# Optimization experiments

Hardware: AMD Instinct MI355X
Metric: run time of the kernel (lower is better)

Reference implementation:

```python
import jax, jax.numpy as jnp
import numpy as np

W, B, S, D = 4, 1, 1024, 1024   # simulated world_size, batch, local seq, embed_dim
H, DS, HM = 16, 64, 4            # num_heads, summary_dim, meta_heads


def mha(q, k, v, w_in, b_in, w_out, b_out, nheads):
    """torch nn.MultiheadAttention (batch_first). Returns (out, head-averaged weights)."""
    d = q.shape[-1]
    hd = d // nheads
    wq, wk, wv = jnp.split(w_in, 3, axis=0)
    bq, bk, bv = jnp.split(b_in, 3)
    Bq, Sq, _ = q.shape
    Sk = k.shape[1]
    qh = (q @ wq.T + bq).reshape(Bq, Sq, nheads, hd)
    kh = (k @ wk.T + bk).reshape(Bq, Sk, nheads, hd)
    vh = (v @ wv.T + bv).reshape(Bq, Sk, nheads, hd)
    scores = jnp.einsum('bqhd,bkhd->bhqk', qh, kh) / float(np.sqrt(hd))
    attn = jax.nn.softmax(scores, axis=-1)
    out = jnp.einsum('bhqk,bkhd->bqhd', attn, vh).reshape(Bq, Sq, d)
    return out @ w_out.T + b_out, attn.mean(axis=1)


def attn_stats(attn):
    """attn: (B, S) -> (B, 4) [entropy, gini, max, top5]."""
    ent = -(attn * jnp.log(attn + 1e-8)).sum(-1, keepdims=True)
    s = jnp.sort(attn, axis=-1)
    n = attn.shape[-1]
    idx = jnp.arange(1, n + 1, dtype=attn.dtype)
    gini = 2.0 * (idx * s).sum(-1) / (n * s.sum(-1) + 1e-8) - (n + 1) / n
    mx = attn.max(-1, keepdims=True)
    k = min(5, n)
    top5 = jax.lax.top_k(attn, k)[0].sum(-1, keepdims=True)
    return jnp.concatenate([ent, gini[..., None], mx, top5], axis=-1)


def _forward(x, local_in_w, local_in_b, local_out_w, local_out_b,
             sum_query, sum_in_w, sum_in_b, sum_out_w, sum_out_b,
             pat_w1, pat_b1, pat_w2, pat_b2, comb_w, comb_b,
             meta_in_w, meta_in_b, meta_out_w, meta_out_b,
             route_w1, route_b1, route_w2, route_b2,
             cross_in_w, cross_in_b, cross_out_w, cross_out_b,
             gate_w, gate_b, proj_w, proj_b):
    nW = x.shape[0]

    # 1) local attention per rank: (W,B,S,D)
    local = jax.vmap(lambda xc: mha(xc, xc, xc, local_in_w, local_in_b,
                                    local_out_w, local_out_b, H)[0])(x)

    # 2) chunk summary per rank
    def summarize(lo):
        q = jnp.broadcast_to(sum_query, (lo.shape[0], 1, lo.shape[-1]))
        content, w = mha(q, lo, lo, sum_in_w, sum_in_b, sum_out_w, sum_out_b, H)
        content, w = content[:, 0], w[:, 0]              # (B,D), (B,S)
        pat = attn_stats(w)                               # (B,4)
        pat = jax.nn.relu(pat @ pat_w1.T + pat_b1) @ pat_w2.T + pat_b2
        return jnp.concatenate([content, pat], axis=-1) @ comb_w.T + comb_b

    summaries = jax.vmap(summarize)(local)                # (W,B,DS)
    all_sum = jnp.transpose(summaries, (1, 0, 2))         # (B,W,DS) = all-gather

    # 3) meta attention over chunk summaries -> routing weights
    refined, chunk_attn = mha(all_sum, all_sum, all_sum,
                              meta_in_w, meta_in_b, meta_out_w, meta_out_b, HM)
    logits = (jax.nn.relu(refined @ route_w1.T + route_b1) @ route_w2.T + route_b2)[..., 0]
    routing = jax.nn.softmax(logits, axis=-1)             # (B,W)

    all_chunks = jnp.transpose(local, (1, 0, 2, 3))       # (B,W,S,D) = all-gather

    # 4) selective cross-attention + gated combine, per rank
    def per_rank(r, lo):
        rm = routing * (1.0 - jax.nn.one_hot(r, nW, dtype=routing.dtype))
        rm = rm / (rm.sum(-1, keepdims=True) + 1e-8)
        kv = jnp.einsum('bw,bwsd->bsd', rm, all_chunks)
        cross, _ = mha(lo, kv, kv, cross_in_w, cross_in_b, cross_out_w, cross_out_b, H)
        g = jax.nn.sigmoid(jnp.concatenate([lo, cross], axis=-1) @ gate_w.T + gate_b)
        comb = g * cross + (1.0 - g) * lo
        return comb @ proj_w.T + proj_b

    out = jax.vmap(per_rank)(jnp.arange(nW), local)       # (W,B,S,D)
    return out


def setup_inputs() -> dict:
    key = jax.random.key(0)
    ks = iter(jax.random.split(key, 40))
    p = lambda *shape: jax.random.normal(next(ks), shape, dtype=jnp.float32) * 0.02
    inp = {
        'x': jax.random.normal(next(ks), (W, B, S, D), dtype=jnp.float32),
        'local_in_w': p(3 * D, D), 'local_in_b': p(3 * D),
        'local_out_w': p(D, D), 'local_out_b': p(D),
        'sum_query': p(1, 1, D),
        'sum_in_w': p(3 * D, D), 'sum_in_b': p(3 * D),
        'sum_out_w': p(D, D), 'sum_out_b': p(D),
        'pat_w1': p(DS, 4), 'pat_b1': p(DS),
        'pat_w2': p(DS, DS), 'pat_b2': p(DS),
        'comb_w': p(DS, D + DS), 'comb_b': p(DS),
        'meta_in_w': p(3 * DS, DS), 'meta_in_b': p(3 * DS),
        'meta_out_w': p(DS, DS), 'meta_out_b': p(DS),
        'route_w1': p(DS, DS), 'route_b1': p(DS),
        'route_w2': p(1, DS), 'route_b2': p(1),
        'cross_in_w': p(3 * D, D), 'cross_in_b': p(3 * D),
        'cross_out_w': p(D, D), 'cross_out_b': p(D),
        'gate_w': p(D, 2 * D), 'gate_b': p(D),
        'proj_w': p(D, D), 'proj_b': p(D),
    }
    return inp


def reference(x, local_in_w, local_in_b, local_out_w, local_out_b,
              sum_query, sum_in_w, sum_in_b, sum_out_w, sum_out_b,
              pat_w1, pat_b1, pat_w2, pat_b2, comb_w, comb_b,
              meta_in_w, meta_in_b, meta_out_w, meta_out_b,
              route_w1, route_b1, route_w2, route_b2,
              cross_in_w, cross_in_b, cross_out_w, cross_out_b,
              gate_w, gate_b, proj_w, proj_b):
    return _forward(x, local_in_w, local_in_b, local_out_w, local_out_b,
                    sum_query, sum_in_w, sum_in_b, sum_out_w, sum_out_b,
                    pat_w1, pat_b1, pat_w2, pat_b2, comb_w, comb_b,
                    meta_in_w, meta_in_b, meta_out_w, meta_out_b,
                    route_w1, route_b1, route_w2, route_b2,
                    cross_in_w, cross_in_b, cross_out_w, cross_out_b,
                    gate_w, gate_b, proj_w, proj_b)
```

## Files before the change

### kernel.cpp

```cpp
#include <hip/hip_runtime.h>
#include <hip/hip_bf16.h>
#include <stdint.h>

typedef uint16_t u16;
typedef __attribute__((ext_vector_type(8))) short short8;
typedef __attribute__((ext_vector_type(4))) short short4v;
typedef __attribute__((ext_vector_type(8))) unsigned short ushort8;
typedef __attribute__((ext_vector_type(4))) float f32x4;

#define AS1 __attribute__((address_space(1)))
#define AS3 __attribute__((address_space(3)))

__device__ __forceinline__ float b2f(u16 u){
  union{uint32_t i; float f;} v; v.i=((uint32_t)u)<<16; return v.f;
}
__device__ __forceinline__ u16 f2b(float f){
  union{uint32_t i; float f;} v; v.f=f;
  return (u16)((v.i + 0x7fffu + ((v.i>>16)&1u))>>16);
}
__device__ __forceinline__ u16 f2bf(float f){
  __hip_bfloat16 h = __float2bfloat16(f);
  return *reinterpret_cast<u16*>(&h);
}

struct CvtP { const float* src[8]; u16* dst[8]; long n[8]; };
__global__ void cvt_multi(CvtP p) {
  const int seg = blockIdx.y;
  const long i = ((long)blockIdx.x*256 + threadIdx.x)*8;
  if (i >= p.n[seg]) return;
  const float* in = p.src[seg];
  float4 a = *(const float4*)&in[i];
  float4 b = *(const float4*)&in[i+4];
  ushort8 o;
  o[0]=f2b(a.x); o[1]=f2b(a.y); o[2]=f2b(a.z); o[3]=f2b(a.w);
  o[4]=f2b(b.x); o[5]=f2b(b.y); o[6]=f2b(b.z); o[7]=f2b(b.w);
  *(ushort8*)&p.dst[seg][i] = o;
}

struct GemmP {
  const u16* A; const u16* B; u16* C; const float* bias;
  const u16* B2; u16* C2; const float* bias2;
  long lda, ldb, ldc, ldb2, ldc2;
  int K, Nstore, Nstore2, ySplit, act, outf;
  float scale;
};

__global__ __launch_bounds__(512) void gemm_nt(GemmP p) {
  __shared__ __align__(16) u16 lA[2][4096];
  __shared__ __align__(16) u16 lB[2][4096];
  const int t = threadIdx.x;
  const int wave = t >> 6, lane = t & 63;
  int by = blockIdx.y;
  const u16* Bp; u16* Cp; const float* bias; long ldb, ldc; int nst;
  if (by >= p.ySplit) {
    by -= p.ySplit; Bp = p.B2; Cp = p.C2; bias = p.bias2;
    ldb = p.ldb2; ldc = p.ldc2; nst = p.Nstore2;
  } else {
    Bp = p.B; Cp = p.C; bias = p.bias; ldb = p.ldb; ldc = p.ldc; nst = p.Nstore;
  }
  const u16* A = p.A + (long)blockIdx.x * 128 * p.lda;
  const u16* B = Bp + (long)by * 128 * ldb;
  const int srow = t >> 2, skk = (t & 3) * 8;
  const int wr = wave >> 2, wc = wave & 3;
  const int fr = lane & 15, fk = (lane >> 4) * 8;
  f32x4 acc[4][2] = {};

  __builtin_amdgcn_global_load_lds((const AS1 void*)(A + (long)srow*p.lda + skk),
                                   (AS3 void*)&lA[0][t*8], 16, 0, 0);
  __builtin_amdgcn_global_load_lds((const AS1 void*)(B + (long)srow*ldb + skk),
                                   (AS3 void*)&lB[0][t*8], 16, 0, 0);
  __syncthreads();
  int cur = 0;
  for (int k0 = 0; k0 < p.K; k0 += 32) {
    if (k0 + 32 < p.K) {
      const int nb = cur ^ 1, kn = k0 + 32;
      __builtin_amdgcn_global_load_lds((const AS1 void*)(A + (long)srow*p.lda + kn + skk),
                                       (AS3 void*)&lA[nb][t*8], 16, 0, 0);
      __builtin_amdgcn_global_load_lds((const AS1 void*)(B + (long)srow*ldb + kn + skk),
                                       (AS3 void*)&lB[nb][t*8], 16, 0, 0);
    }
    short8 av[4], bv[2];
    #pragma unroll
    for (int mi = 0; mi < 4; ++mi) av[mi] = *(const short8*)&lA[cur][(wr*64 + mi*16 + fr)*32 + fk];
    #pragma unroll
    for (int ni = 0; ni < 2; ++ni) bv[ni] = *(const short8*)&lB[cur][(wc*32 + ni*16 + fr)*32 + fk];
    #pragma unroll
    for (int mi = 0; mi < 4; ++mi)
      #pragma unroll
      for (int ni = 0; ni < 2; ++ni)
        acc[mi][ni] = __builtin_amdgcn_mfma_f32_16x16x32_bf16(av[mi], bv[ni], acc[mi][ni], 0, 0, 0);
    __syncthreads();
    cur ^= 1;
  }

  const int rbase = blockIdx.x*128 + wr*64;
  const int cbase = by*128 + wc*32;
  const int rsub = (lane >> 4) * 4;
  #pragma unroll
  for (int ni = 0; ni < 2; ++ni) {
    const int col = cbase + ni*16 + fr;
    if (col >= nst) continue;
    const float bs = bias ? bias[col] : 0.f;
    #pragma unroll
    for (int mi = 0; mi < 4; ++mi) {
      #pragma unroll
      for (int j = 0; j < 4; ++j) {
        float v = acc[mi][ni][j] * p.scale + bs;
        if (p.act == 1) v = 1.f / (1.f + __expf(-v));
        const long idx = (long)(rbase + mi*16 + rsub + j) * ldc + col;
        if (p.outf) ((float*)Cp)[idx] = v;
        else        Cp[idx] = f2b(v);
      }
    }
  }
}

struct FlashP {
  const u16 *q, *k, *v; u16* o;
  long ldq, ldkv, ldo;
  long qB, kvB, oB;
};

__global__ __launch_bounds__(256) void flash_k(FlashP p) {
  const int t = threadIdx.x, w4 = t >> 6, lane = t & 63;
  const int qt = blockIdx.x, h = blockIdx.y, wz = blockIdx.z;
  const int fr = lane & 15, g = lane >> 4, fk = g * 8;
  __shared__ __align__(16) u16 kt[64][72];
  __shared__ __align__(16) u16 vt[64][72];
  __shared__ __align__(16) u16 pl[4][16][72];

  const u16* Q = p.q + (long)wz*p.qB + (long)(qt*64 + w4*16)*p.ldq + h*64;
  const u16* K = p.k + (long)wz*p.kvB + h*64;
  const u16* V = p.v + (long)wz*p.kvB + h*64;

  short8 aq[2];
  aq[0] = *(const short8*)&Q[(long)fr*p.ldq + fk];
  aq[1] = *(const short8*)&Q[(long)fr*p.ldq + 32 + fk];

  f32x4 acc[4] = {};
  float ml = -3e38f, ll = 0.f;
  const float C = 0.125f * 1.44269504f;

  const int krow = t >> 2, kseg = (t & 3) * 16;
  const int vp = t & 31, vc = (t >> 5) * 8;

  short8 kr0, kr1, vr0, vr1;
  kr0 = *(const short8*)&K[(long)krow*p.ldkv + kseg];
  kr1 = *(const short8*)&K[(long)krow*p.ldkv + kseg + 8];
  vr0 = *(const short8*)&V[(long)(2*vp)*p.ldkv + vc];
  vr1 = *(const short8*)&V[(long)(2*vp + 1)*p.ldkv + vc];

  for (int it = 0; it < 16; ++it) {
    *(short8*)&kt[krow][kseg]     = kr0;
    *(short8*)&kt[krow][kseg + 8] = kr1;
    #pragma unroll
    for (int e = 0; e < 8; ++e) {
      const uint32_t pk = (uint32_t)(uint16_t)vr0[e] | ((uint32_t)(uint16_t)vr1[e] << 16);
      *(uint32_t*)&vt[vc + e][2*vp] = pk;
    }
    __syncthreads();

    if (it + 1 < 16) {
      const int kn = (it + 1) * 64;
      kr0 = *(const short8*)&K[(long)(kn + krow)*p.ldkv + kseg];
      kr1 = *(const short8*)&K[(long)(kn + krow)*p.ldkv + kseg + 8];
      vr0 = *(const short8*)&V[(long)(kn + 2*vp)*p.ldkv + vc];
      vr1 = *(const short8*)&V[(long)(kn + 2*vp + 1)*p.ldkv + vc];
    }

    f32x4 s[4] = {};
    __builtin_amdgcn_s_setprio(1);
    #pragma unroll
    for (int ni = 0; ni < 4; ++ni) {
      short8 bk0 = *(const short8*)&kt[ni*16 + fr][fk];
      short8 bk1 = *(const short8*)&kt[ni*16 + fr][32 + fk];
      s[ni] = __builtin_amdgcn_mfma_f32_16x16x32_bf16(bk0, aq[0], s[ni], 0, 0, 0);
      s[ni] = __builtin_amdgcn_mfma_f32_16x16x32_bf16(bk1, aq[1], s[ni], 0, 0, 0);
    }
    __builtin_amdgcn_s_setprio(0);

    float rm = s[0][0];
    #pragma unroll
    for (int ni = 0; ni < 4; ++ni)
      #pragma unroll
      for (int j = 0; j < 4; ++j) rm = fmaxf(rm, s[ni][j]);
    rm = fmaxf(rm, __shfl_xor(rm, 16, 64));
    rm = fmaxf(rm, __shfl_xor(rm, 32, 64));
    const float rml = rm * C;

    if (__any(rml > ml + 11.5f)) {
      const float mnl = fmaxf(ml, rml);
      const float al = exp2f(ml - mnl);
      const float a0 = __shfl(al, g*4 + 0, 64);
      const float a1 = __shfl(al, g*4 + 1, 64);
      const float a2 = __shfl(al, g*4 + 2, 64);
      const float a3 = __shfl(al, g*4 + 3, 64);
      #pragma unroll
      for (int nv = 0; nv < 4; ++nv) {
        acc[nv][0] *= a0; acc[nv][1] *= a1; acc[nv][2] *= a2; acc[nv][3] *= a3;
      }
      ll *= al;
      ml = mnl;
    }

    float rs = 0.f;
    u16 pb[4][4];
    #pragma unroll
    for (int ni = 0; ni < 4; ++ni)
      #pragma unroll
      for (int j = 0; j < 4; ++j) {
        const float pv = exp2f(s[ni][j]*C - ml);
        rs += pv;
        pb[ni][j] = f2bf(pv);
      }
    rs += __shfl_xor(rs, 16, 64);
    rs += __shfl_xor(rs, 32, 64);
    ll += rs;

    #pragma unroll
    for (int ni = 0; ni < 4; ++ni) {
      short4v pk4;
      pk4[0] = (short)pb[ni][0]; pk4[1] = (short)pb[ni][1];
      pk4[2] = (short)pb[ni][2]; pk4[3] = (short)pb[ni][3];
      *(short4v*)&pl[w4][fr][ni*16 + g*4] = pk4;
    }

    __builtin_amdgcn_s_setprio(1);
    #pragma unroll
    for (int ks = 0; ks < 2; ++ks) {
      short8 pa = *(const short8*)&pl[w4][fr][ks*32 + fk];
      #pragma unroll
      for (int nv = 0; nv < 4; ++nv) {
        short8 bvv = *(const short8*)&vt[nv*16 + fr][ks*32 + fk];
        acc[nv] = __builtin_amdgcn_mfma_f32_16x16x32_bf16(pa, bvv, acc[nv], 0, 0, 0);
      }
    }
    __builtin_amdgcn_s_setprio(0);
    __syncthreads();
  }

  const float l0 = __shfl(ll, g*4 + 0, 64);
  const float l1 = __shfl(ll, g*4 + 1, 64);
  const float l2 = __shfl(ll, g*4 + 2, 64);
  const float l3 = __shfl(ll, g*4 + 3, 64);
  const float inv[4] = {1.f/l0, 1.f/l1, 1.f/l2, 1.f/l3};
  u16* O = p.o + (long)wz*p.oB + (long)(qt*64 + w4*16)*p.ldo + h*64;
  #pragma unroll
  for (int j = 0; j < 4; ++j)
    #pragma unroll
    for (int nv = 0; nv < 4; ++nv)
      O[(long)(g*4 + j)*p.ldo + nv*16 + fr] = f2bf(acc[nv][j] * inv[j]);
}

__global__ void gemv_qs(const float* sq, const float* w, const float* b, float* out) {
  const int t = threadIdx.x, nl = t & 63, kq = t >> 6;
  const int n = blockIdx.x*64 + nl;
  const float* row = w + (long)n * 1024 + kq*256;
  const float* q = sq + kq*256;
  float s = 0.f;
  for (int k = 0; k < 256; k += 4) {
    float4 ww = *(const float4*)&row[k];
    float4 qq = *(const float4*)&q[k];
    s += qq.x*ww.x + qq.y*ww.y + qq.z*ww.z + qq.w*ww.w;
  }
  __shared__ float ps[4][64];
  ps[kq][nl] = s;
  __syncthreads();
  if (t < 64) out[blockIdx.x*64 + t] = ps[0][t]+ps[1][t]+ps[2][t]+ps[3][t] + b[blockIdx.x*64 + t];
}

__global__ void sum_attend(const float* qs, const u16* sumkv, float* content, float* pall) {
  const int h = blockIdx.x, w = blockIdx.y, t = threadIdx.x;
  const int lane = t & 63, wv = t >> 6;
  __shared__ float qsh[64];
  __shared__ float sc[1024];
  __shared__ float rmax[4], rsum[4];
  __shared__ float po[4][64];
  if (t < 64) qsh[t] = qs[h*64 + t];
  __syncthreads();
  const u16* kbase = sumkv + (long)w*2097152 + h*64;
  float e[4];
  float mx = -1e30f;
  #pragma unroll
  for (int j = 0; j < 4; ++j) {
    const int k = j*256 + t;
    const u16* krow = kbase + (long)k * 2048;
    float s = 0.f;
    #pragma unroll
    for (int d = 0; d < 64; d += 8) {
      ushort8 kk = *(const ushort8*)&krow[d];
      #pragma unroll
      for (int q = 0; q < 8; ++q) s += qsh[d+q] * b2f(kk[q]);
    }
    s *= 0.125f;
    e[j] = s;
    mx = fmaxf(mx, s);
  }
  #pragma unroll
  for (int o = 32; o; o >>= 1) mx = fmaxf(mx, __shfl_xor(mx, o, 64));
  if (lane == 0) rmax[wv] = mx;
  __syncthreads();
  mx = fmaxf(fmaxf(rmax[0],rmax[1]), fmaxf(rmax[2],rmax[3]));
  float sum = 0.f;
  #pragma unroll
  for (int j = 0; j < 4; ++j) { e[j] = __expf(e[j]-mx); sum += e[j]; }
  #pragma unroll
  for (int o = 32; o; o >>= 1) sum += __shfl_xor(sum, o, 64);
  if (lane == 0) rsum[wv] = sum;
  __syncthreads();
  const float inv = 1.f / (rsum[0]+rsum[1]+rsum[2]+rsum[3]);
  float* pr = pall + ((long)w*16 + h)*1024;
  #pragma unroll
  for (int j = 0; j < 4; ++j) {
    const int k = j*256 + t;
    const float pn = e[j]*inv;
    sc[k] = pn;
    pr[k] = pn;
  }
  __syncthreads();
  const u16* vbase = sumkv + (long)w*2097152 + 1024 + h*64;
  float o = 0.f;
  const int k0 = wv*256;
  for (int k = k0; k < k0+256; ++k) o += sc[k] * b2f(vbase[(long)k*2048 + lane]);
  po[wv][lane] = o;
  __syncthreads();
  if (t < 64) content[(long)w*1024 + h*64 + t] = po[0][t]+po[1][t]+po[2][t]+po[3][t];
}

__global__ void wavg_k(const float* pall, float* wavg) {
  const int w = blockIdx.y, k = blockIdx.x*256 + threadIdx.x;
  float s = 0.f;
  #pragma unroll
  for (int h = 0; h < 16; ++h) s += pall[((long)w*16 + h)*1024 + k];
  wavg[w*1024 + k] = s * (1.f/16.f);
}

__global__ void contproj_k(const float* content, const float* w_, const float* b, float* out) {
  const int w = blockIdx.y, t = threadIdx.x;
  const int nl = t & 63, kq = t >> 6;
  const int n = blockIdx.x*64 + nl;
  const float* c = content + w*1024 + kq*256;
  const float* row = w_ + (long)n * 1024 + kq*256;
  float s = 0.f;
  for (int k = 0; k < 256; k += 4) {
    float4 ww = *(const float4*)&row[k];
    s += c[k]*ww.x + c[k+1]*ww.y + c[k+2]*ww.z + c[k+3]*ww.w;
  }
  __shared__ float ps[4][64];
  ps[kq][nl] = s;
  __syncthreads();
  if (t < 64) out[w*1024 + blockIdx.x*64 + t] = ps[0][t]+ps[1][t]+ps[2][t]+ps[3][t] + b[blockIdx.x*64 + t];
}

__global__ void stats1_k(const float* wavg, float* part) {
  const int c = blockIdx.x, w = blockIdx.y, t = threadIdx.x;
  __shared__ float a[1024];
  for (int i = t; i < 1024; i += 256) a[i] = wavg[w*1024 + i];
  __syncthreads();
  const int jl = t & 63, iq = t >> 6;
  const int j = c*64 + jl;
  const float aj = a[j];
  int pr = 0;
  const int i0 = iq*256;
  #pragma unroll 8
  for (int i = i0; i < i0+256; ++i) {
    const float ai = a[i];
    pr += (ai < aj) || (ai == aj && i < j);
  }
  __shared__ int prs[4][64];
  prs[iq][jl] = pr;
  __syncthreads();
  if (t < 64) {
    const int rank = 1 + prs[0][jl] + prs[1][jl] + prs[2][jl] + prs[3][jl];
    float ent = -aj * logf(aj + 1e-8f);
    float gnum = (float)rank * aj;
    float ssum = aj;
    float mx = aj;
    float top5 = (rank >= 1020) ? aj : 0.f;
    #pragma unroll
    for (int o = 32; o; o >>= 1) {
      ent += __shfl_xor(ent, o, 64);
      gnum += __shfl_xor(gnum, o, 64);
      ssum += __shfl_xor(ssum, o, 64);
      mx = fmaxf(mx, __shfl_xor(mx, o, 64));
      top5 += __shfl_xor(top5, o, 64);
    }
    if (t == 0) {
      float* pp = part + ((w*16 + c) * 5);
      pp[0]=ent; pp[1]=gnum; pp[2]=ssum; pp[3]=mx; pp[4]=top5;
    }
  }
}

__global__ void stats2_k(const float* part, float* stats) {
  const int w = blockIdx.x, t = threadIdx.x;
  const int c = t & 15, stat = t >> 4;
  float v = 0.f;
  const bool active = stat < 5;
  if (active) v = part[(w*16 + c)*5 + stat];
  #pragma unroll
  for (int o = 8; o; o >>= 1) {
    const float ov = __shfl_xor(v, o, 64);
    v = (stat == 3) ? fmaxf(v, ov) : (v + ov);
  }
  __shared__ float r5[5];
  if (active && c == 0) r5[stat] = v;
  __syncthreads();
  if (t == 0) {
    stats[w*4+0] = r5[0];
    stats[w*4+1] = 2.f*r5[1]/(1024.f*r5[2] + 1e-8f) - 1025.f/1024.f;
    stats[w*4+2] = r5[3];
    stats[w*4+3] = r5[4];
  }
}

__global__ void patsum_k(const float* stats, const float* contprj,
                         const float* pw1, const float* pb1, const float* pw2, const float* pb2,
                         const float* combw, const float* combb, float* summ) {
  const int w = blockIdx.x, t = threadIdx.x;
  const int nl = t & 63, kq = t >> 6;
  __shared__ float p1[64], pat[64];
  __shared__ float ps[4][64];
  __shared__ float ps2[4][64];
  if (t < 64) {
    float s = 0.f;
    #pragma unroll
    for (int k = 0; k < 4; ++k) s += stats[w*4+k] * pw1[t*4+k];
    p1[t] = fmaxf(s + pb1[t], 0.f);
  }
  __syncthreads();
  {
    float s = 0.f;
    const float* rw = pw2 + (long)nl*64 + kq*16;
    const float* pp = p1 + kq*16;
    #pragma unroll
    for (int k = 0; k < 16; ++k) s += pp[k] * rw[k];
    ps[kq][nl] = s;
  }
  __syncthreads();
  if (t < 64) pat[t] = ps[0][t]+ps[1][t]+ps[2][t]+ps[3][t] + pb2[t];
  __syncthreads();
  const float* c = contprj + w*1024;
  const float* row = combw + (long)nl * 1088;
  float s = 0.f;
  const int k0 = kq*272;
  for (int k = k0; k < k0+272; ++k) {
    const float rv = row[k];
    const float cv = (k < 1024) ? c[k] : pat[k-1024];
    s += cv * rv;
  }
  ps2[kq][nl] = s;
  __syncthreads();
  if (t < 64) summ[w*64 + t] = ps2[0][t]+ps2[1][t]+ps2[2][t]+ps2[3][t] + combb[t];
}

__global__ void meta_k(const float* summ, const float* miw, const float* mib,
                       const float* mow, const float* mob, const float* rw1, const float* rb1,
                       const float* rw2, const float* rb2, float* routing) {
  const int t = threadIdx.x;
  __shared__ float qkv[4][192];
  __shared__ float sc[64];
  __shared__ float o[4][64];
  __shared__ float rf[4][64];
  __shared__ float t1[4][64];
  __shared__ float lg[4];
  for (int idx = t; idx < 768; idx += 64) {
    const int w = idx / 192, rrow = idx % 192;
    const float* rw = miw + (long)rrow * 64;
    float s = 0.f;
    for (int k = 0; k < 64; ++k) s += summ[w*64+k] * rw[k];
    qkv[w][rrow] = s + mib[rrow];
  }
  __syncthreads();
  {
    const int h = t >> 4, i = (t >> 2) & 3, j = t & 3;
    float s = 0.f;
    #pragma unroll
    for (int d = 0; d < 16; ++d) s += qkv[i][h*16+d] * qkv[j][64 + h*16+d];
    sc[t] = s * 0.25f;
  }
  __syncthreads();
  if (t < 16) {
    const float a0=sc[t*4], a1=sc[t*4+1], a2=sc[t*4+2], a3=sc[t*4+3];
    const float m = fmaxf(fmaxf(a0,a1), fmaxf(a2,a3));
    const float e0=__expf(a0-m), e1=__expf(a1-m), e2=__expf(a2-m), e3=__expf(a3-m);
    const float s = e0+e1+e2+e3;
    sc[t*4]=e0/s; sc[t*4+1]=e1/s; sc[t*4+2]=e2/s; sc[t*4+3]=e3/s;
  }
  __syncthreads();
  for (int idx = t; idx < 256; idx += 64) {
    const int i = idx >> 6, c = idx & 63, h = c >> 4;
    float s = 0.f;
    #pragma unroll
    for (int j = 0; j < 4; ++j) s += sc[(h*4+i)*4+j] * qkv[j][128 + c];
    o[i][c] = s;
  }
  __syncthreads();
  for (int idx = t; idx < 256; idx += 64) {
    const int i = idx >> 6, n = idx & 63;
    const float* rw = mow + (long)n * 64;
    float s = 0.f;
    for (int k = 0; k < 64; ++k) s += o[i][k] * rw[k];
    rf[i][n] = s + mob[n];
  }
  __syncthreads();
  for (int idx = t; idx < 256; idx += 64) {
    const int i = idx >> 6, n = idx & 63;
    const float* rw = rw1 + (long)n * 64;
    float s = 0.f;
    for (int k = 0; k < 64; ++k) s += rf[i][k] * rw[k];
    t1[i][n] = fmaxf(s + rb1[n], 0.f);
  }
  __syncthreads();
  if (t < 4) {
    float s = 0.f;
    for (int k = 0; k < 64; ++k) s += t1[t][k] * rw2[k];
    lg[t] = s + rb2[0];
  }
  __syncthreads();
  if (t == 0) {
    const float m = fmaxf(fmaxf(lg[0],lg[1]), fmaxf(lg[2],lg[3]));
    float e[4], s = 0.f;
    #pragma unroll
    for (int i = 0; i < 4; ++i) { e[i] = __expf(lg[i]-m); s += e[i]; }
    #pragma unroll
    for (int i = 0; i < 4; ++i) routing[i] = e[i]/s;
  }
}

__global__ void kvr_k(const u16* local, const float* routing, u16* kvr) {
  const int r = blockIdx.y;
  const long e = ((long)blockIdx.x*256 + threadIdx.x) * 8;
  float rm[4]; float s = 0.f;
  #pragma unroll
  for (int w = 0; w < 4; ++w) { rm[w] = (w == r) ? 0.f : routing[w]; s += rm[w]; }
  const float inv = 1.f / (s + 1e-8f);
  ushort8 a0 = *(const ushort8*)&local[e];
  ushort8 a1 = *(const ushort8*)&local[1048576 + e];
  ushort8 a2 = *(const ushort8*)&local[2097152 + e];
  ushort8 a3 = *(const ushort8*)&local[3145728 + e];
  ushort8 out;
  #pragma unroll
  for (int j = 0; j < 8; ++j)
    out[j] = f2b((rm[0]*b2f(a0[j]) + rm[1]*b2f(a1[j]) + rm[2]*b2f(a2[j]) + rm[3]*b2f(a3[j])) * inv);
  *(ushort8*)&kvr[(long)r*1048576 + e] = out;
}

__global__ void gcat_k(const u16* local, const u16* cross, u16* gcat) {
  const long e = ((long)blockIdx.x*256 + threadIdx.x) * 8;
  const long row = e >> 11, col = e & 2047;
  const u16* src = (col < 1024) ? &local[row*1024 + col] : &cross[row*1024 + col - 1024];
  *(ushort8*)&gcat[e] = *(const ushort8*)src;
}

__global__ void comb_k(const u16* g, const u16* cross, const u16* local, u16* comb) {
  const long e = ((long)blockIdx.x*256 + threadIdx.x) * 8;
  ushort8 gg = *(const ushort8*)&g[e];
  ushort8 cc = *(const ushort8*)&cross[e];
  ushort8 ll = *(const ushort8*)&local[e];
  ushort8 out;
  #pragma unroll
  for (int j = 0; j < 8; ++j) {
    const float gf = b2f(gg[j]);
    out[j] = f2b(gf*b2f(cc[j]) + (1.f-gf)*b2f(ll[j]));
  }
  *(ushort8*)&comb[e] = out;
}

static void gemm1(hipStream_t st, dim3 grid,
                  const u16* A, long lda, const u16* B, long ldb,
                  u16* C, long ldc, const float* bias,
                  int K, int N, float scale, int act, int outf) {
  GemmP p = {};
  p.A=A; p.B=B; p.C=C; p.bias=bias;
  p.lda=lda; p.ldb=ldb; p.ldc=ldc;
  p.K=K; p.Nstore=N; p.ySplit=1<<30; p.act=act; p.outf=outf; p.scale=scale;
  gemm_nt<<<grid, dim3(512), 0, st>>>(p);
}

extern "C" void kernel_launch(void* const* d_in, const int* in_sizes, int n_in,
                              void* d_out, int out_size, void* d_ws, size_t ws_size,
                              hipStream_t stream) {
  (void)in_sizes; (void)n_in; (void)out_size; (void)ws_size;
  const float* x   = (const float*)d_in[0];
  const float* liw = (const float*)d_in[1];
  const float* lib = (const float*)d_in[2];
  const float* low = (const float*)d_in[3];
  const float* lob = (const float*)d_in[4];
  const float* sq  = (const float*)d_in[5];
  const float* siw = (const float*)d_in[6];
  const float* sib = (const float*)d_in[7];
  const float* sow = (const float*)d_in[8];
  const float* sob = (const float*)d_in[9];
  const float* pw1 = (const float*)d_in[10];
  const float* pb1 = (const float*)d_in[11];
  const float* pw2 = (const float*)d_in[12];
  const float* pb2 = (const float*)d_in[13];
  const float* cbw = (const float*)d_in[14];
  const float* cbb = (const float*)d_in[15];
  const float* miw = (const float*)d_in[16];
  const float* mib = (const float*)d_in[17];
  const float* mow = (const float*)d_in[18];
  const float* mob = (const float*)d_in[19];
  const float* rw1 = (const float*)d_in[20];
  const float* rb1 = (const float*)d_in[21];
  const float* rw2 = (const float*)d_in[22];
  const float* rb2 = (const float*)d_in[23];
  const float* ciw = (const float*)d_in[24];
  const float* cib = (const float*)d_in[25];
  const float* cow = (const float*)d_in[26];
  const float* cob = (const float*)d_in[27];
  const float* gw  = (const float*)d_in[28];
  const float* gb  = (const float*)d_in[29];
  const float* pw  = (const float*)d_in[30];
  const float* pb  = (const float*)d_in[31];

  char* ws = (char*)d_ws;
  u16* qkv    = (u16*)(ws + 0);
  u16* aout   = (u16*)(ws + 25165824);
  u16* local  = (u16*)(ws + 33554432);
  u16* scratch= (u16*)(ws + 41943040);
  u16* s2048  = (u16*)(ws + 79691776);
  u16* cq     = (u16*)(ws + 96468992);
  u16* kvr    = (u16*)(ws + 104857600);
  u16* crossb = (u16*)(ws + 113246208);
  char* sf = ws + 121634816;
  float* qs      = (float*)(sf + 0);
  float* pall    = (float*)(sf + 4096);
  float* wavg    = (float*)(sf + 266240);
  float* content = (float*)(sf + 282624);
  float* contprj = (float*)(sf + 299008);
  float* stats   = (float*)(sf + 315392);
  float* summ    = (float*)(sf + 315456);
  float* routing = (float*)(sf + 316480);
  float* part    = (float*)(sf + 316544);
  u16* siwkvb = (u16*)(ws + 122028032);
  u16* lowb   = (u16*)(ws + 126222336);
  u16* ciwb   = (u16*)(ws + 128319488);
  u16* cowb   = (u16*)(ws + 134610944);
  u16* gwb    = (u16*)(ws + 136708096);
  u16* pwb    = (u16*)(ws + 140902400);
  u16* xb   = crossb;
  u16* liwb = scratch;

  CvtP cp;
  cp.src[0]=x;   cp.dst[0]=xb;     cp.n[0]=4194304;
  cp.src[1]=liw; cp.dst[1]=liwb;   cp.n[1]=3145728;
  cp.src[2]=low; cp.dst[2]=lowb;   cp.n[2]=1048576;
  cp.src[3]=siw+1048576; cp.dst[3]=siwkvb; cp.n[3]=2097152;
  cp.src[4]=ciw; cp.dst[4]=ciwb;   cp.n[4]=3145728;
  cp.src[5]=cow; cp.dst[5]=cowb;   cp.n[5]=1048576;
  cp.src[6]=gw;  cp.dst[6]=gwb;    cp.n[6]=2097152;
  cp.src[7]=pw;  cp.dst[7]=pwb;    cp.n[7]=1048576;
  cvt_multi<<<dim3(2048, 8), dim3(256), 0, stream>>>(cp);

  gemm1(stream, dim3(32,24), xb,1024, liwb,1024, qkv,3072, lib, 1024, 3072, 1.f, 0, 0);

  {
    FlashP fp;
    fp.q = qkv; fp.k = qkv + 1024; fp.v = qkv + 2048; fp.o = aout;
    fp.ldq = 3072; fp.ldkv = 3072; fp.ldo = 1024;
    fp.qB = 3145728; fp.kvB = 3145728; fp.oB = 1048576;
    flash_k<<<dim3(16,16,4), dim3(256), 0, stream>>>(fp);
  }

  gemm1(stream, dim3(32,8), aout,1024, lowb,1024, local,1024, lob, 1024, 1024, 1.f, 0, 0);

  {
    GemmP p = {};
    p.A = local; p.lda = 1024; p.K = 1024; p.scale = 1.f;
    p.B = ciwb;   p.C = cq;    p.bias = cib;      p.ldb = 1024; p.ldc = 1024; p.Nstore = 1024;
    p.B2 = siwkvb; p.C2 = s2048; p.bias2 = sib+1024; p.ldb2 = 1024; p.ldc2 = 2048; p.Nstore2 = 2048;
    p.ySplit = 8;
    gemm_nt<<<dim3(32,24), dim3(512), 0, stream>>>(p);
  }

  gemv_qs<<<dim3(16), dim3(256), 0, stream>>>(sq, siw, sib, qs);
  sum_attend<<<dim3(16,4), dim3(256), 0, stream>>>(qs, s2048, content, pall);
  wavg_k<<<dim3(4,4), dim3(256), 0, stream>>>(pall, wavg);
  contproj_k<<<dim3(16,4), dim3(256), 0, stream>>>(content, sow, sob, contprj);
  stats1_k<<<dim3(16,4), dim3(256), 0, stream>>>(wavg, part);
  stats2_k<<<dim3(4), dim3(128), 0, stream>>>(part, stats);
  patsum_k<<<dim3(4), dim3(256), 0, stream>>>(stats, contprj, pw1, pb1, pw2, pb2, cbw, cbb, summ);

  meta_k<<<dim3(1), dim3(64), 0, stream>>>(summ, miw, mib, mow, mob, rw1, rb1, rw2, rb2, routing);

  kvr_k<<<dim3(512,4), dim3(256), 0, stream>>>(local, routing, kvr);

  gemm1(stream, dim3(32,16), kvr,1024, ciwb+1048576,1024, s2048,2048, cib+1024, 1024, 2048, 1.f, 0, 0);

  {
    FlashP fp;
    fp.q = cq; fp.k = s2048; fp.v = s2048 + 1024; fp.o = aout;
    fp.ldq = 1024; fp.ldkv = 2048; fp.ldo = 1024;
    fp.qB = 1048576; fp.kvB = 2097152; fp.oB = 1048576;
    flash_k<<<dim3(16,16,4), dim3(256), 0, stream>>>(fp);
  }

  gemm1(stream, dim3(32,8), aout,1024, cowb,1024, crossb,1024, cob, 1024, 1024, 1.f, 0, 0);

  gcat_k<<<dim3(4096), dim3(256), 0, stream>>>(local, crossb, s2048);
  gemm1(stream, dim3(32,8), s2048,2048, gwb,2048, cq,1024, gb, 2048, 1024, 1.f, 1, 0);

  comb_k<<<dim3(2048), dim3(256), 0, stream>>>(cq, crossb, local, kvr);

  gemm1(stream, dim3(32,8), kvr,1024, pwb,1024, (u16*)d_out,1024, pb, 1024, 1024, 1.f, 0, 1);
}
```

Measured before the change: 433.2 us.

## Fuse gate concat and combine into GEMM; process two query fragments per flash wave

The gate GEMM now reads its two K-halves straight from the local and cross buffers, so the concat kernel is no longer needed. A new epilogue mode applies the sigmoid and the gated blend of cross and local in place, which removes the separate combine kernel and its round trips through memory. Separately, each flash-attention wave now handles 32 query rows (two 16-row fragments), so each K/V tile loaded into LDS is reused twice and the grid is halved. The cost is higher register pressure in the attention kernel and fewer blocks per launch.

```diff
diff --git a/kernel.cpp b/kernel.cpp
--- a/kernel.cpp
+++ b/kernel.cpp
@@ -40,6 +40,7 @@
 struct GemmP {
   const u16* A; const u16* B; u16* C; const float* bias;
   const u16* B2; u16* C2; const float* bias2;
+  const u16* A2; const u16* lr; const u16* cr;
   long lda, ldb, ldc, ldb2, ldc2;
   int K, Nstore, Nstore2, ySplit, act, outf;
   float scale;
@@ -58,39 +59,43 @@
   } else {
     Bp = p.B; Cp = p.C; bias = p.bias; ldb = p.ldb; ldc = p.ldc; nst = p.Nstore;
   }
-  const u16* A = p.A + (long)blockIdx.x * 128 * p.lda;
   const u16* B = Bp + (long)by * 128 * ldb;
   const int srow = t >> 2, skk = (t & 3) * 8;
   const int wr = wave >> 2, wc = wave & 3;
   const int fr = lane & 15, fk = (lane >> 4) * 8;
   f32x4 acc[4][2] = {};
 
-  __builtin_amdgcn_global_load_lds((const AS1 void*)(A + (long)srow*p.lda + skk),
-                                   (AS3 void*)&lA[0][t*8], 16, 0, 0);
-  __builtin_amdgcn_global_load_lds((const AS1 void*)(B + (long)srow*ldb + skk),
-                                   (AS3 void*)&lB[0][t*8], 16, 0, 0);
-  __syncthreads();
+  const int nseg = p.A2 ? 2 : 1;
   int cur = 0;
-  for (int k0 = 0; k0 < p.K; k0 += 32) {
-    if (k0 + 32 < p.K) {
-      const int nb = cur ^ 1, kn = k0 + 32;
-      __builtin_amdgcn_global_load_lds((const AS1 void*)(A + (long)srow*p.lda + kn + skk),
-                                       (AS3 void*)&lA[nb][t*8], 16, 0, 0);
-      __builtin_amdgcn_global_load_lds((const AS1 void*)(B + (long)srow*ldb + kn + skk),
-                                       (AS3 void*)&lB[nb][t*8], 16, 0, 0);
-    }
-    short8 av[4], bv[2];
-    #pragma unroll
-    for (int mi = 0; mi < 4; ++mi) av[mi] = *(const short8*)&lA[cur][(wr*64 + mi*16 + fr)*32 + fk];
-    #pragma unroll
-    for (int ni = 0; ni < 2; ++ni) bv[ni] = *(const short8*)&lB[cur][(wc*32 + ni*16 + fr)*32 + fk];
-    #pragma unroll
-    for (int mi = 0; mi < 4; ++mi)
-      #pragma unroll
-      for (int ni = 0; ni < 2; ++ni)
-        acc[mi][ni] = __builtin_amdgcn_mfma_f32_16x16x32_bf16(av[mi], bv[ni], acc[mi][ni], 0, 0, 0);
+  for (int seg = 0; seg < nseg; ++seg) {
+    const u16* A = (seg ? p.A2 : p.A) + (long)blockIdx.x * 128 * p.lda;
+    const u16* Bs = B + (long)seg * p.K;
+    __builtin_amdgcn_global_load_lds((const AS1 void*)(A + (long)srow*p.lda + skk),
+                                     (AS3 void*)&lA[cur][t*8], 16, 0, 0);
+    __builtin_amdgcn_global_load_lds((const AS1 void*)(Bs + (long)srow*ldb + skk),
+                                     (AS3 void*)&lB[cur][t*8], 16, 0, 0);
     __syncthreads();
-    cur ^= 1;
+    for (int k0 = 0; k0 < p.K; k0 += 32) {
+      if (k0 + 32 < p.K) {
+        const int nb = cur ^ 1, kn = k0 + 32;
+        __builtin_amdgcn_global_load_lds((const AS1 void*)(A + (long)srow*p.lda + kn + skk),
+                                         (AS3 void*)&lA[nb][t*8], 16, 0, 0);
+        __builtin_amdgcn_global_load_lds((const AS1 void*)(Bs + (long)srow*ldb + kn + skk),
+                                         (AS3 void*)&lB[nb][t*8], 16, 0, 0);
+      }
+      short8 av[4], bv[2];
+      #pragma unroll
+      for (int mi = 0; mi < 4; ++mi) av[mi] = *(const short8*)&lA[cur][(wr*64 + mi*16 + fr)*32 + fk];
+      #pragma unroll
+      for (int ni = 0; ni < 2; ++ni) bv[ni] = *(const short8*)&lB[cur][(wc*32 + ni*16 + fr)*32 + fk];
+      #pragma unroll
+      for (int mi = 0; mi < 4; ++mi)
+        #pragma unroll
+        for (int ni = 0; ni < 2; ++ni)
+          acc[mi][ni] = __builtin_amdgcn_mfma_f32_16x16x32_bf16(av[mi], bv[ni], acc[mi][ni], 0, 0, 0);
+      __syncthreads();
+      cur ^= 1;
+    }
   }
 
   const int rbase = blockIdx.x*128 + wr*64;
@@ -106,10 +111,17 @@
       #pragma unroll
       for (int j = 0; j < 4; ++j) {
         float v = acc[mi][ni][j] * p.scale + bs;
-        if (p.act == 1) v = 1.f / (1.f + __expf(-v));
         const long idx = (long)(rbase + mi*16 + rsub + j) * ldc + col;
-        if (p.outf) ((float*)Cp)[idx] = v;
-        else        Cp[idx] = f2b(v);
+        if (p.act == 2) {
+          const float gv = 1.f / (1.f + __expf(-v));
+          const float cv = b2f(p.cr[idx]);
+          const float lv = b2f(p.lr[idx]);
+          Cp[idx] = f2b(gv*cv + (1.f - gv)*lv);
+        } else {
+          if (p.act == 1) v = 1.f / (1.f + __expf(-v));
+          if (p.outf) ((float*)Cp)[idx] = v;
+          else        Cp[idx] = f2b(v);
+        }
       }
     }
   }
@@ -127,18 +139,21 @@
   const int fr = lane & 15, g = lane >> 4, fk = g * 8;
   __shared__ __align__(16) u16 kt[64][72];
   __shared__ __align__(16) u16 vt[64][72];
-  __shared__ __align__(16) u16 pl[4][16][72];
-
-  const u16* Q = p.q + (long)wz*p.qB + (long)(qt*64 + w4*16)*p.ldq + h*64;
+  __shared__ __align__(16) u16 pl[4][32][72];
+
+  const u16* Q = p.q + (long)wz*p.qB + (long)(qt*128 + w4*32)*p.ldq + h*64;
   const u16* K = p.k + (long)wz*p.kvB + h*64;
   const u16* V = p.v + (long)wz*p.kvB + h*64;
 
-  short8 aq[2];
-  aq[0] = *(const short8*)&Q[(long)fr*p.ldq + fk];
-  aq[1] = *(const short8*)&Q[(long)fr*p.ldq + 32 + fk];
-
-  f32x4 acc[4] = {};
-  float ml = -3e38f, ll = 0.f;
+  short8 aq[2][2];
+  #pragma unroll
+  for (int f = 0; f < 2; ++f) {
+    aq[f][0] = *(const short8*)&Q[(long)(f*16 + fr)*p.ldq + fk];
+    aq[f][1] = *(const short8*)&Q[(long)(f*16 + fr)*p.ldq + 32 + fk];
+  }
+
+  f32x4 acc[2][4] = {};
+  float ml[2] = {-3e38f, -3e38f}, ll[2] = {0.f, 0.f};
   const float C = 0.125f * 1.44269504f;
 
   const int krow = t >> 2, kseg = (t & 3) * 16;
@@ -168,88 +183,100 @@
       vr1 = *(const short8*)&V[(long)(kn + 2*vp + 1)*p.ldkv + vc];
     }
 
-    f32x4 s[4] = {};
+    f32x4 s[2][4] = {};
     __builtin_amdgcn_s_setprio(1);
     #pragma unroll
     for (int ni = 0; ni < 4; ++ni) {
       short8 bk0 = *(const short8*)&kt[ni*16 + fr][fk];
       short8 bk1 = *(const short8*)&kt[ni*16 + fr][32 + fk];
-      s[ni] = __builtin_amdgcn_mfma_f32_16x16x32_bf16(bk0, aq[0], s[ni], 0, 0, 0);
-      s[ni] = __builtin_amdgcn_mfma_f32_16x16x32_bf16(bk1, aq[1], s[ni], 0, 0, 0);
+      #pragma unroll
+      for (int f = 0; f < 2; ++f) {
+        s[f][ni] = __builtin_amdgcn_mfma_f32_16x16x32_bf16(bk0, aq[f][0], s[f][ni], 0, 0, 0);
+        s[f][ni] = __builtin_amdgcn_mfma_f32_16x16x32_bf16(bk1, aq[f][1], s[f][ni], 0, 0, 0);
+      }
     }
     __builtin_amdgcn_s_setprio(0);
 
-    float rm = s[0][0];
-    #pragma unroll
-    for (int ni = 0; ni < 4; ++ni)
-      #pragma unroll
-      for (int j = 0; j < 4; ++j) rm = fmaxf(rm, s[ni][j]);
-    rm = fmaxf(rm, __shfl_xor(rm, 16, 64));
-    rm = fmaxf(rm, __shfl_xor(rm, 32, 64));
-    const float rml = rm * C;
-
-    if (__any(rml > ml + 11.5f)) {
-      const float mnl = fmaxf(ml, rml);
-      const float al = exp2f(ml - mnl);
-      const float a0 = __shfl(al, g*4 + 0, 64);
-      const float a1 = __shfl(al, g*4 + 1, 64);
-      const float a2 = __shfl(al, g*4 + 2, 64);
-      const float a3 = __shfl(al, g*4 + 3, 64);
-      #pragma unroll
-      for (int nv = 0; nv < 4; ++nv) {
-        acc[nv][0] *= a0; acc[nv][1] *= a1; acc[nv][2] *= a2; acc[nv][3] *= a3;
+    #pragma unroll
+    for (int f = 0; f < 2; ++f) {
+      float rm = s[f][0][0];
+      #pragma unroll
+      for (int ni = 0; ni < 4; ++ni)
+        #pragma unroll
+        for (int j = 0; j < 4; ++j) rm = fmaxf(rm, s[f][ni][j]);
+      rm = fmaxf(rm, __shfl_xor(rm, 16, 64));
+      rm = fmaxf(rm, __shfl_xor(rm, 32, 64));
+      const float rml = rm * C;
+
+      if (__any(rml > ml[f] + 11.5f)) {
+        const float mnl = fmaxf(ml[f], rml);
+        const float al = exp2f(ml[f] - mnl);
+        const float a0 = __shfl(al, g*4 + 0, 64);
+        const float a1 = __shfl(al, g*4 + 1, 64);
+        const float a2 = __shfl(al, g*4 + 2, 64);
+        const float a3 = __shfl(al, g*4 + 3, 64);
+        #pragma unroll
+        for (int nv = 0; nv < 4; ++nv) {
+          acc[f][nv][0] *= a0; acc[f][nv][1] *= a1;
+          acc[f][nv][2] *= a2; acc[f][nv][3] *= a3;
+        }
+        ll[f] *= al;
+        ml[f] = mnl;
       }
-      ll *= al;
-      ml = mnl;
-    }
-
-    float rs = 0.f;
-    u16 pb[4][4];
-    #pragma unroll
-    for (int ni = 0; ni < 4; ++ni)
-      #pragma unroll
-      for (int j = 0; j < 4; ++j) {
-        const float pv = exp2f(s[ni][j]*C - ml);
-        rs += pv;
-        pb[ni][j] = f2bf(pv);
+
+      float rs = 0.f;
+      u16 pb[4][4];
+      #pragma unroll
+      for (int ni = 0; ni < 4; ++ni)
+        #pragma unroll
+        for (int j = 0; j < 4; ++j) {
+          const float pv = exp2f(s[f][ni][j]*C - ml[f]);
+          rs += pv;
+          pb[ni][j] = f2bf(pv);
+        }
+      rs += __shfl_xor(rs, 16, 64);
+      rs += __shfl_xor(rs, 32, 64);
+      ll[f] += rs;
+
+      #pragma unroll
+      for (int ni = 0; ni < 4; ++ni) {
+        short4v pk4;
+        pk4[0] = (short)pb[ni][0]; pk4[1] = (short)pb[ni][1];
+        pk4[2] = (short)pb[ni][2]; pk4[3] = (short)pb[ni][3];
+        *(short4v*)&pl[w4][f*16 + fr][ni*16 + g*4] = pk4;
       }
-    rs += __shfl_xor(rs, 16, 64);
-    rs += __shfl_xor(rs, 32, 64);
-    ll += rs;
-
-    #pragma unroll
-    for (int ni = 0; ni < 4; ++ni) {
-      short4v pk4;
-      pk4[0] = (short)pb[ni][0]; pk4[1] = (short)pb[ni][1];
-      pk4[2] = (short)pb[ni][2]; pk4[3] = (short)pb[ni][3];
-      *(short4v*)&pl[w4][fr][ni*16 + g*4] = pk4;
     }
 
     __builtin_amdgcn_s_setprio(1);
     #pragma unroll
     for (int ks = 0; ks < 2; ++ks) {
-      short8 pa = *(const short8*)&pl[w4][fr][ks*32 + fk];
+      short8 pa0 = *(const short8*)&pl[w4][fr][ks*32 + fk];
+      short8 pa1 = *(const short8*)&pl[w4][16 + fr][ks*32 + fk];
       #pragma unroll
       for (int nv = 0; nv < 4; ++nv) {
         short8 bvv = *(const short8*)&vt[nv*16 + fr][ks*32 + fk];
-        acc[nv] = __builtin_amdgcn_mfma_f32_16x16x32_bf16(pa, bvv, acc[nv], 0, 0, 0);
+        acc[0][nv] = __builtin_amdgcn_mfma_f32_16x16x32_bf16(pa0, bvv, acc[0][nv], 0, 0, 0);
+        acc[1][nv] = __builtin_amdgcn_mfma_f32_16x16x32_bf16(pa1, bvv, acc[1][nv], 0, 0, 0);
       }
     }
     __builtin_amdgcn_s_setprio(0);
     __syncthreads();
   }
 
-  const float l0 = __shfl(ll, g*4 + 0, 64);
-  const float l1 = __shfl(ll, g*4 + 1, 64);
-  const float l2 = __shfl(ll, g*4 + 2, 64);
-  const float l3 = __shfl(ll, g*4 + 3, 64);
-  const float inv[4] = {1.f/l0, 1.f/l1, 1.f/l2, 1.f/l3};
-  u16* O = p.o + (long)wz*p.oB + (long)(qt*64 + w4*16)*p.ldo + h*64;
-  #pragma unroll
-  for (int j = 0; j < 4; ++j)
-    #pragma unroll
-    for (int nv = 0; nv < 4; ++nv)
-      O[(long)(g*4 + j)*p.ldo + nv*16 + fr] = f2bf(acc[nv][j] * inv[j]);
+  u16* O = p.o + (long)wz*p.oB + (long)(qt*128 + w4*32)*p.ldo + h*64;
+  #pragma unroll
+  for (int f = 0; f < 2; ++f) {
+    const float l0 = __shfl(ll[f], g*4 + 0, 64);
+    const float l1 = __shfl(ll[f], g*4 + 1, 64);
+    const float l2 = __shfl(ll[f], g*4 + 2, 64);
+    const float l3 = __shfl(ll[f], g*4 + 3, 64);
+    const float inv[4] = {1.f/l0, 1.f/l1, 1.f/l2, 1.f/l3};
+    #pragma unroll
+    for (int j = 0; j < 4; ++j)
+      #pragma unroll
+      for (int nv = 0; nv < 4; ++nv)
+        O[(long)(f*16 + g*4 + j)*p.ldo + nv*16 + fr] = f2bf(acc[f][nv][j] * inv[j]);
+  }
 }
 
 __global__ void gemv_qs(const float* sq, const float* w, const float* b, float* out) {
@@ -544,27 +571,6 @@
   for (int j = 0; j < 8; ++j)
     out[j] = f2b((rm[0]*b2f(a0[j]) + rm[1]*b2f(a1[j]) + rm[2]*b2f(a2[j]) + rm[3]*b2f(a3[j])) * inv);
   *(ushort8*)&kvr[(long)r*1048576 + e] = out;
-}
-
-__global__ void gcat_k(const u16* local, const u16* cross, u16* gcat) {
-  const long e = ((long)blockIdx.x*256 + threadIdx.x) * 8;
-  const long row = e >> 11, col = e & 2047;
-  const u16* src = (col < 1024) ? &local[row*1024 + col] : &cross[row*1024 + col - 1024];
-  *(ushort8*)&gcat[e] = *(const ushort8*)src;
-}
-
-__global__ void comb_k(const u16* g, const u16* cross, const u16* local, u16* comb) {
-  const long e = ((long)blockIdx.x*256 + threadIdx.x) * 8;
-  ushort8 gg = *(const ushort8*)&g[e];
-  ushort8 cc = *(const ushort8*)&cross[e];
-  ushort8 ll = *(const ushort8*)&local[e];
-  ushort8 out;
-  #pragma unroll
-  for (int j = 0; j < 8; ++j) {
-    const float gf = b2f(gg[j]);
-    out[j] = f2b(gf*b2f(cc[j]) + (1.f-gf)*b2f(ll[j]));
-  }
-  *(ushort8*)&comb[e] = out;
 }
 
 static void gemm1(hipStream_t st, dim3 grid,
@@ -661,7 +667,7 @@
     fp.q = qkv; fp.k = qkv + 1024; fp.v = qkv + 2048; fp.o = aout;
     fp.ldq = 3072; fp.ldkv = 3072; fp.ldo = 1024;
     fp.qB = 3145728; fp.kvB = 3145728; fp.oB = 1048576;
-    flash_k<<<dim3(16,16,4), dim3(256), 0, stream>>>(fp);
+    flash_k<<<dim3(8,16,4), dim3(256), 0, stream>>>(fp);
   }
 
   gemm1(stream, dim3(32,8), aout,1024, lowb,1024, local,1024, lob, 1024, 1024, 1.f, 0, 0);
@@ -694,15 +700,19 @@
     fp.q = cq; fp.k = s2048; fp.v = s2048 + 1024; fp.o = aout;
     fp.ldq = 1024; fp.ldkv = 2048; fp.ldo = 1024;
     fp.qB = 1048576; fp.kvB = 2097152; fp.oB = 1048576;
-    flash_k<<<dim3(16,16,4), dim3(256), 0, stream>>>(fp);
+    flash_k<<<dim3(8,16,4), dim3(256), 0, stream>>>(fp);
   }
 
   gemm1(stream, dim3(32,8), aout,1024, cowb,1024, crossb,1024, cob, 1024, 1024, 1.f, 0, 0);
 
-  gcat_k<<<dim3(4096), dim3(256), 0, stream>>>(local, crossb, s2048);
-  gemm1(stream, dim3(32,8), s2048,2048, gwb,2048, cq,1024, gb, 2048, 1024, 1.f, 1, 0);
-
-  comb_k<<<dim3(2048), dim3(256), 0, stream>>>(cq, crossb, local, kvr);
+  {
+    GemmP p = {};
+    p.A = local; p.A2 = crossb; p.lr = local; p.cr = crossb;
+    p.B = gwb; p.C = kvr; p.bias = gb;
+    p.lda = 1024; p.ldb = 2048; p.ldc = 1024;
+    p.K = 1024; p.Nstore = 1024; p.ySplit = 1<<30; p.act = 2; p.outf = 0; p.scale = 1.f;
+    gemm_nt<<<dim3(32,8), dim3(512), 0, stream>>>(p);
+  }
 
   gemm1(stream, dim3(32,8), kvr,1024, pwb,1024, (u16*)d_out,1024, pb, 1024, 1024, 1.f, 0, 1);
 }
```

New measurement: 428.2 us. Within noise of the previous version (-1.2%).
